# Optimization experiments

Measured on AMD Instinct MI355X. Metric: run time of the kernel, lower is better.

Reference implementation:

```python
import jax, jax.numpy as jnp
import numpy as np

N_NODES = 50000
N_EDGES = 800000
N_GRAPHS = 128
IN_DIM = 12          # state_ndim + action_ndim
C = 64               # n_channels
N_LAYERS = 2
NEG_SLOPE = 0.01     # torch leaky_relu default


def setup_inputs() -> dict:
    key = jax.random.key(0)
    ks = jax.random.split(key, 16)
    state = jax.random.normal(ks[0], (N_NODES, 8), dtype=jnp.float32)
    action = jax.random.normal(ks[1], (N_NODES, 4), dtype=jnp.float32)
    edge_index = jax.random.randint(ks[2], (2, N_EDGES), 0, N_NODES, dtype=jnp.int64)
    edge_attr = jax.random.normal(ks[3], (N_EDGES, IN_DIM), dtype=jnp.float32)
    batch = jnp.sort(jax.random.randint(ks[4], (N_NODES,), 0, N_GRAPHS, dtype=jnp.int64))
    s = 0.05
    params = {
        "W_in": jax.random.normal(ks[5], (IN_DIM, C), dtype=jnp.float32) * s,
        "b_in": jnp.zeros((C,), dtype=jnp.float32),
        "W_self": jax.random.normal(ks[6], (N_LAYERS, C, C), dtype=jnp.float32) * s,
        "W_nbr": jax.random.normal(ks[7], (N_LAYERS, C, C), dtype=jnp.float32) * s,
        "W_edge": jax.random.normal(ks[8], (N_LAYERS, IN_DIM, C), dtype=jnp.float32) * s,
        "b_conv": jnp.zeros((N_LAYERS, C), dtype=jnp.float32),
        "W_out": jax.random.normal(ks[9], (C, 1), dtype=jnp.float32) * s,
        "b_out": jnp.zeros((1,), dtype=jnp.float32),
    }
    return {"state": state, "action": action, "edge_index": edge_index,
            "edge_attr": edge_attr, "batch": batch, **params}


def reference(state, action, edge_index, edge_attr, batch,
              W_in, b_in, W_self, W_nbr, W_edge, b_conv, W_out, b_out):
    N = state.shape[0]
    src, dst = edge_index[0], edge_index[1]
    act = lambda v: jax.nn.leaky_relu(v, NEG_SLOPE)

    # read-in: concat state/action -> node embedding [N, C]
    x = jnp.concatenate([state, action], axis=-1)
    h = act(x @ W_in + b_in)

    # message passing: gather -> transform -> scatter-add, edge_attr-conditioned
    for l in range(W_self.shape[0]):
        m = h[src] @ W_nbr[l] + edge_attr @ W_edge[l]          # [E, C]
        agg = jax.ops.segment_sum(m, dst, num_segments=N)      # [N, C]
        h = act(h @ W_self[l] + agg + b_conv[l])

    # read-out to scalar per node, then scatter_mean over graph ids
    y = h @ W_out + b_out                                      # [N, 1]
    sums = jax.ops.segment_sum(y, batch, num_segments=N_GRAPHS)
    counts = jax.ops.segment_sum(jnp.ones((N, 1), y.dtype), batch,
                                 num_segments=N_GRAPHS)
    return sums / jnp.maximum(counts, 1.0)                     # [B, 1]
```

## Files before the change

### kernel.cpp

```cpp
#include <hip/hip_runtime.h>

#define NN 50000
#define NE 800000
#define NG 128
#define IN_DIM 12
#define C 64
#define KTOT 160
#define NEG_SLOPE 0.01f
#define SCAN_BLOCKS 196
#define NOWN 8
#define OWN_RANGE 6250
#define ESTRIPE 2048
#define NSTRIPES ((NE + ESTRIPE - 1) / ESTRIPE)

typedef short short8 __attribute__((ext_vector_type(8)));
typedef float f32x4 __attribute__((ext_vector_type(4)));
typedef unsigned int uint4v __attribute__((ext_vector_type(4)));

__device__ __forceinline__ float lrelu(float v) {
    return v > 0.f ? v : NEG_SLOPE * v;
}
__device__ __forceinline__ float bflo(uint32_t v) { return __uint_as_float(v << 16); }
__device__ __forceinline__ float bfhi(uint32_t v) { return __uint_as_float(v & 0xffff0000u); }
__device__ __forceinline__ unsigned short bf16r(float x) {
    uint32_t u = __float_as_uint(x);
    u += 0x7fffu + ((u >> 16) & 1u);
    return (unsigned short)(u >> 16);
}
__device__ __forceinline__ uint32_t pack_bf16(float lo, float hi) {
    return (uint32_t)bf16r(lo) | ((uint32_t)bf16r(hi) << 16);
}

__global__ void readin_kernel(const float* __restrict__ state,
                              const float* __restrict__ action,
                              const float* __restrict__ W_in,
                              const float* __restrict__ b_in,
                              uint32_t* __restrict__ hb) {
    __shared__ float sW[IN_DIM * C];
    __shared__ float sb[C];
    int tid = threadIdx.x;
    for (int i = tid; i < IN_DIM * C; i += blockDim.x) sW[i] = W_in[i];
    if (tid < C) sb[tid] = b_in[tid];
    __syncthreads();

    int node = blockIdx.x * (blockDim.x >> 6) + (tid >> 6);
    int c = tid & 63;
    if (node >= NN) return;

    float x[IN_DIM];
#pragma unroll
    for (int k = 0; k < 8; k++) x[k] = state[node * 8 + k];
#pragma unroll
    for (int k = 0; k < 4; k++) x[8 + k] = action[node * 4 + k];

    float acc = sb[c];
#pragma unroll
    for (int k = 0; k < IN_DIM; k++) acc += x[k] * sW[k * C + c];
    float res = lrelu(acc);
    float p = __shfl_xor(res, 1);
    if (!(c & 1)) hb[node * 32 + (c >> 1)] = pack_bf16(res, p);
}

__global__ void hist_part(const int* __restrict__ dst, int* __restrict__ deg) {
    int owner = blockIdx.x & (NOWN - 1);
    int stripe = blockIdx.x >> 3;
    int lo = owner * OWN_RANGE, hi = lo + OWN_RANGE;
    int base = stripe * ESTRIPE;
    int end = base + ESTRIPE; if (end > NE) end = NE;
    for (int e = base + threadIdx.x; e < end; e += 256) {
        int d = dst[e];
        if (d >= lo && d < hi) atomicAdd(&deg[d], 1);
    }
}

__global__ void scan1_kernel(const int* __restrict__ deg,
                             int* __restrict__ excl,
                             int* __restrict__ bsum) {
    __shared__ int tmp[256];
    int tid = threadIdx.x;
    int i = blockIdx.x * 256 + tid;
    int v = (i < NN) ? deg[i] : 0;
    tmp[tid] = v;
    __syncthreads();
    for (int off = 1; off < 256; off <<= 1) {
        int t = (tid >= off) ? tmp[tid - off] : 0;
        __syncthreads();
        tmp[tid] += t;
        __syncthreads();
    }
    if (i < NN) excl[i] = tmp[tid] - v;
    if (tid == 255) bsum[blockIdx.x] = tmp[255];
}

__global__ void scan23_kernel(const int* __restrict__ excl,
                              const int* __restrict__ bsum,
                              int* __restrict__ row_start,
                              int* __restrict__ cursor) {
    __shared__ int s_off;
    int tid = threadIdx.x;
    if (tid < 64) {
        int p = 0;
        for (int i = tid; i < blockIdx.x; i += 64) p += bsum[i];
#pragma unroll
        for (int off = 32; off; off >>= 1) p += __shfl_xor(p, off);
        if (tid == 0) s_off = p;
    }
    __syncthreads();
    int i = blockIdx.x * 256 + tid;
    if (i < NN) {
        int v = excl[i] + s_off;
        row_start[i] = v;
        cursor[i] = v;
    }
}

__global__ void fill_part(const int* __restrict__ src,
                          const int* __restrict__ dst,
                          const float* __restrict__ edge_attr,
                          int* __restrict__ cursor,
                          int* __restrict__ csr_src,
                          uint4v* __restrict__ csr_ea) {
    int owner = blockIdx.x & (NOWN - 1);
    int stripe = blockIdx.x >> 3;
    int lo = owner * OWN_RANGE, hi = lo + OWN_RANGE;
    int base = stripe * ESTRIPE;
    int end = base + ESTRIPE; if (end > NE) end = NE;
    for (int e = base + threadIdx.x; e < end; e += 256) {
        int d = dst[e];
        if (d >= lo && d < hi) {
            int slot = atomicAdd(&cursor[d], 1);
            csr_src[slot] = src[e];
            const float4* ea = reinterpret_cast<const float4*>(edge_attr + e * IN_DIM);
            float4 f0 = ea[0], f1 = ea[1], f2 = ea[2];
            uint4v w0, w1;
            w0[0] = pack_bf16(f0.x, f0.y); w0[1] = pack_bf16(f0.z, f0.w);
            w0[2] = pack_bf16(f1.x, f1.y); w0[3] = pack_bf16(f1.z, f1.w);
            w1[0] = pack_bf16(f2.x, f2.y); w1[1] = pack_bf16(f2.z, f2.w);
            w1[2] = 0u; w1[3] = 0u;
            csr_ea[slot * 2] = w0;
            csr_ea[slot * 2 + 1] = w1;
        }
    }
}

__global__ void wprep_kernel(const float* __restrict__ W_self,
                             const float* __restrict__ W_nbr,
                             const float* __restrict__ W_edge,
                             unsigned short* __restrict__ WT) {
    int idx = blockIdx.x * 256 + threadIdx.x;
    if (idx >= 2 * C * KTOT) return;
    int l = idx / (C * KTOT);
    int rem = idx % (C * KTOT);
    int col = rem / KTOT;
    int k = rem % KTOT;
    float v = 0.f;
    if (k < C)                    v = W_self[l * C * C + k * C + col];
    else if (k < 2 * C)           v = W_nbr[l * C * C + (k - C) * C + col];
    else if (k < 2 * C + IN_DIM)  v = W_edge[l * IN_DIM * C + (k - 2 * C) * C + col];
    WT[idx] = bf16r(v);
}

__global__ void agg_e_kernel(const uint32_t* __restrict__ csr_ea,
                             const int* __restrict__ row_start,
                             const int* __restrict__ deg,
                             uint32_t* __restrict__ aggeb) {
    int tid = threadIdx.x;
    int node = blockIdx.x * (blockDim.x >> 6) + (tid >> 6);
    int lane = tid & 63;
    if (node >= NN) return;
    int start = row_start[node], cnt = deg[node];
    int eg = lane >> 3;
    int comp = lane & 7;
    float s0 = 0.f, s1 = 0.f;
    for (int j = eg; j < cnt; j += 8) {
        uint32_t v = csr_ea[(size_t)(start + j) * 8 + comp];
        s0 += bflo(v); s1 += bfhi(v);
    }
    s0 += __shfl_xor(s0, 8);  s1 += __shfl_xor(s1, 8);
    s0 += __shfl_xor(s0, 16); s1 += __shfl_xor(s1, 16);
    s0 += __shfl_xor(s0, 32); s1 += __shfl_xor(s1, 32);
    if (lane < 8) aggeb[node * 8 + comp] = pack_bf16(s0, s1);
}

__global__ void gather_kernel(const uint32_t* __restrict__ hb_in,
                              const int* __restrict__ row_start,
                              const int* __restrict__ deg,
                              const int* __restrict__ csr_src,
                              uint32_t* __restrict__ aggb) {
    int tid = threadIdx.x;
    int node = blockIdx.x * (blockDim.x >> 6) + (tid >> 6);
    int lane = tid & 63;
    if (node >= NN) return;

    int start = row_start[node], cnt = deg[node];
    int half = lane >> 5;
    int q = lane & 31;

    int myidx = (lane < cnt) ? csr_src[start + lane] : 0;
    int nb = cnt < 64 ? cnt : 64;

    float a0 = 0.f, a1 = 0.f, b0v = 0.f, b1v = 0.f;
    float c0 = 0.f, c1 = 0.f, d0 = 0.f, d1 = 0.f;
    int j = 0;
    for (; j + 16 <= nb; j += 16) {
        int p = j + 4 * half;
        int s0 = __shfl(myidx, p);
        int s1 = __shfl(myidx, p + 1);
        int s2 = __shfl(myidx, p + 2);
        int s3 = __shfl(myidx, p + 3);
        int s4 = __shfl(myidx, p + 8);
        int s5 = __shfl(myidx, p + 9);
        int s6 = __shfl(myidx, p + 10);
        int s7 = __shfl(myidx, p + 11);
        uint32_t v0 = hb_in[s0 * 32 + q];
        uint32_t v1 = hb_in[s1 * 32 + q];
        uint32_t v2 = hb_in[s2 * 32 + q];
        uint32_t v3 = hb_in[s3 * 32 + q];
        uint32_t v4 = hb_in[s4 * 32 + q];
        uint32_t v5 = hb_in[s5 * 32 + q];
        uint32_t v6 = hb_in[s6 * 32 + q];
        uint32_t v7 = hb_in[s7 * 32 + q];
        a0  += bflo(v0); a1  += bfhi(v0);
        b0v += bflo(v1); b1v += bfhi(v1);
        c0  += bflo(v2); c1  += bfhi(v2);
        d0  += bflo(v3); d1  += bfhi(v3);
        a0  += bflo(v4); a1  += bfhi(v4);
        b0v += bflo(v5); b1v += bfhi(v5);
        c0  += bflo(v6); c1  += bfhi(v6);
        d0  += bflo(v7); d1  += bfhi(v7);
    }
    for (; j + 8 <= nb; j += 8) {
        int p = j + 4 * half;
        int s0 = __shfl(myidx, p);
        int s1 = __shfl(myidx, p + 1);
        int s2 = __shfl(myidx, p + 2);
        int s3 = __shfl(myidx, p + 3);
        uint32_t v0 = hb_in[s0 * 32 + q];
        uint32_t v1 = hb_in[s1 * 32 + q];
        uint32_t v2 = hb_in[s2 * 32 + q];
        uint32_t v3 = hb_in[s3 * 32 + q];
        a0  += bflo(v0); a1  += bfhi(v0);
        b0v += bflo(v1); b1v += bfhi(v1);
        c0  += bflo(v2); c1  += bfhi(v2);
        d0  += bflo(v3); d1  += bfhi(v3);
    }
    for (; j + 2 <= nb; j += 2) {
        int s = __shfl(myidx, j + half);
        uint32_t v = hb_in[s * 32 + q];
        a0 += bflo(v); a1 += bfhi(v);
    }
    {
        int s = __shfl(myidx, (j < 64) ? j : 0);
        if (j < nb && half == 0) {
            uint32_t v = hb_in[s * 32 + q];
            a0 += bflo(v); a1 += bfhi(v);
        }
    }
    for (int i2 = 64 + half; i2 < cnt; i2 += 2) {
        int s = csr_src[start + i2];
        uint32_t v = hb_in[s * 32 + q];
        a0 += bflo(v); a1 += bfhi(v);
    }
    a0 += b0v + c0 + d0;
    a1 += b1v + c1 + d1;
    a0 += __shfl_xor(a0, 32);
    a1 += __shfl_xor(a1, 32);
    if (lane < 32) aggb[node * 32 + q] = pack_bf16(a0, a1);
}

__global__ __launch_bounds__(512) void gemm_kernel(
        const uint32_t* __restrict__ hbA,
        const uint32_t* __restrict__ aggb,
        const uint32_t* __restrict__ aggeb,
        const unsigned short* __restrict__ WT,
        const float* __restrict__ bias,
        unsigned short* __restrict__ hb_out) {
    int tid = threadIdx.x;
    int w = tid >> 6;
    int l = tid & 63;
    int mt = blockIdx.x * 2 + (w >> 2);
    if (mt * 16 >= NN) return;
    int nt = w & 3;
    int node_base = mt * 16;

    int arow = l & 15;
    int kg = l >> 4;
    int gcol = nt * 16 + arow;

    const uint32_t* aptr = hbA + (node_base + arow) * 32 + kg * 4;
    const uint32_t* gptr = aggb + (node_base + arow) * 32 + kg * 4;
    short8 a0 = __builtin_bit_cast(short8, *reinterpret_cast<const uint4v*>(aptr));
    short8 a1 = __builtin_bit_cast(short8, *reinterpret_cast<const uint4v*>(aptr + 16));
    short8 a2 = __builtin_bit_cast(short8, *reinterpret_cast<const uint4v*>(gptr));
    short8 a3 = __builtin_bit_cast(short8, *reinterpret_cast<const uint4v*>(gptr + 16));
    short8 a4 = {0, 0, 0, 0, 0, 0, 0, 0};
    if (kg < 2)
        a4 = __builtin_bit_cast(short8, *reinterpret_cast<const uint4v*>(
                 aggeb + (node_base + arow) * 8 + kg * 4));

    const unsigned short* bbase = WT + gcol * KTOT + kg * 8;
    short8 b0 = __builtin_bit_cast(short8, *reinterpret_cast<const uint4v*>(bbase));
    short8 b1 = __builtin_bit_cast(short8, *reinterpret_cast<const uint4v*>(bbase + 32));
    short8 b2 = __builtin_bit_cast(short8, *reinterpret_cast<const uint4v*>(bbase + 64));
    short8 b3 = __builtin_bit_cast(short8, *reinterpret_cast<const uint4v*>(bbase + 96));
    short8 b4 = __builtin_bit_cast(short8, *reinterpret_cast<const uint4v*>(bbase + 128));

    float bv = bias[gcol];
    f32x4 acc = {bv, bv, bv, bv};

    acc = __builtin_amdgcn_mfma_f32_16x16x32_bf16(a0, b0, acc, 0, 0, 0);
    acc = __builtin_amdgcn_mfma_f32_16x16x32_bf16(a1, b1, acc, 0, 0, 0);
    acc = __builtin_amdgcn_mfma_f32_16x16x32_bf16(a2, b2, acc, 0, 0, 0);
    acc = __builtin_amdgcn_mfma_f32_16x16x32_bf16(a3, b3, acc, 0, 0, 0);
    acc = __builtin_amdgcn_mfma_f32_16x16x32_bf16(a4, b4, acc, 0, 0, 0);

#pragma unroll
    for (int r = 0; r < 4; r++) {
        float res = lrelu(acc[r]);
        hb_out[(node_base + kg * 4 + r) * C + gcol] = bf16r(res);
    }
}

__global__ void readout_fused(const unsigned short* __restrict__ hb,
                              const float* __restrict__ W_out,
                              const float* __restrict__ b_out,
                              const int* __restrict__ batch,
                              float* __restrict__ sums,
                              float* __restrict__ counts) {
    __shared__ float s_sum[NG];
    __shared__ float s_cnt[NG];
    int tid = threadIdx.x;
    if (tid < NG) { s_sum[tid] = 0.f; s_cnt[tid] = 0.f; }
    __syncthreads();

    int lane = tid & 63;
    int wave = tid >> 6;
    int base = blockIdx.x * 256 + wave * 64;
    float w = W_out[lane];
    float b0 = b_out[0];

    if (base < NN) {
        int last = base + 63;
        bool full = (last < NN);
        int gf = batch[base];
        int gl = batch[full ? last : (NN - 1)];
        if (full && gf == gl) {
            float p = 0.f;
            for (int i = 0; i < 64; i++)
                p += __uint_as_float((uint32_t)hb[(base + i) * C + lane] << 16);
            p *= w;
#pragma unroll
            for (int off = 32; off; off >>= 1) p += __shfl_xor(p, off);
            if (lane == 0) {
                atomicAdd(&s_sum[gf], p + 64.f * b0);
                atomicAdd(&s_cnt[gf], 64.f);
            }
        } else {
            float y_local = 0.f;
            for (int i = 0; i < 64; i++) {
                int nd = base + i;
                float v = 0.f;
                if (nd < NN) v = __uint_as_float((uint32_t)hb[nd * C + lane] << 16) * w;
#pragma unroll
                for (int off = 32; off; off >>= 1) v += __shfl_xor(v, off);
                if (lane == i) y_local = v + b0;
            }
            int nd = base + lane;
            if (nd < NN) {
                int g = batch[nd];
                atomicAdd(&s_sum[g], y_local);
                atomicAdd(&s_cnt[g], 1.0f);
            }
        }
    }
    __syncthreads();
    if (tid < NG && s_cnt[tid] != 0.f) {
        atomicAdd(&sums[tid], s_sum[tid]);
        atomicAdd(&counts[tid], s_cnt[tid]);
    }
}

__global__ void finalize_kernel(const float* __restrict__ sums,
                                const float* __restrict__ counts,
                                float* __restrict__ out) {
    int g = threadIdx.x;
    if (g < NG) out[g] = sums[g] / fmaxf(counts[g], 1.0f);
}

extern "C" void kernel_launch(void* const* d_in, const int* in_sizes, int n_in,
                              void* d_out, int out_size, void* d_ws, size_t ws_size,
                              hipStream_t stream) {
    const float* state     = (const float*)d_in[0];
    const float* action    = (const float*)d_in[1];
    const int*   edge_index= (const int*)d_in[2];
    const float* edge_attr = (const float*)d_in[3];
    const int*   batch     = (const int*)d_in[4];
    const float* W_in      = (const float*)d_in[5];
    const float* b_in      = (const float*)d_in[6];
    const float* W_self    = (const float*)d_in[7];
    const float* W_nbr     = (const float*)d_in[8];
    const float* W_edge    = (const float*)d_in[9];
    const float* b_conv    = (const float*)d_in[10];
    const float* W_out     = (const float*)d_in[11];
    const float* b_out     = (const float*)d_in[12];
    float* out = (float*)d_out;

    const int* src = edge_index;
    const int* dst = edge_index + NE;

    float* ws      = (float*)d_ws;
    float* sums    = ws;
    float* counts  = sums + NG;
    int*   deg     = (int*)(counts + NG);
    int*   excl    = deg + NN;
    int*   row_start = excl + NN;
    int*   cursor  = row_start + NN;
    int*   bsum    = cursor + NN;
    int*   csr_src = bsum + 256;
    uint32_t* csr_ea = (uint32_t*)(csr_src + NE);
    uint32_t* hb_a = csr_ea + (size_t)NE * 8;
    uint32_t* hb_b = hb_a + NN * 32;
    uint32_t* aggb = hb_b + NN * 32;
    uint32_t* aggeb = aggb + NN * 32;
    unsigned short* WT = (unsigned short*)(aggeb + NN * 8);

    hipMemsetAsync(deg, 0, NN * sizeof(int), stream);
    hipMemsetAsync(sums, 0, 2 * NG * sizeof(float), stream);

    const int THREADS = 256;
    int node_blocks = (NN + 3) / 4;
    int part_blocks = NSTRIPES * NOWN;

    readin_kernel<<<node_blocks, THREADS, 0, stream>>>(state, action, W_in, b_in, hb_a);

    hist_part<<<part_blocks, THREADS, 0, stream>>>(dst, deg);
    scan1_kernel<<<SCAN_BLOCKS, 256, 0, stream>>>(deg, excl, bsum);
    scan23_kernel<<<SCAN_BLOCKS, 256, 0, stream>>>(excl, bsum, row_start, cursor);
    fill_part<<<part_blocks, THREADS, 0, stream>>>(src, dst, edge_attr, cursor,
                                                   csr_src, (uint4v*)csr_ea);

    wprep_kernel<<<80, 256, 0, stream>>>(W_self, W_nbr, W_edge, WT);

    agg_e_kernel<<<node_blocks, THREADS, 0, stream>>>(csr_ea, row_start, deg, aggeb);

    int gemm_blocks = (3125 + 1) / 2;

    gather_kernel<<<node_blocks, THREADS, 0, stream>>>(hb_a, row_start, deg, csr_src, aggb);
    gemm_kernel<<<gemm_blocks, 512, 0, stream>>>(
        hb_a, aggb, aggeb, WT, b_conv, (unsigned short*)hb_b);

    gather_kernel<<<node_blocks, THREADS, 0, stream>>>(hb_b, row_start, deg, csr_src, aggb);
    gemm_kernel<<<gemm_blocks, 512, 0, stream>>>(
        hb_b, aggb, aggeb, WT + C * KTOT, b_conv + C, (unsigned short*)hb_a);

    int ro_blocks = (NN + 255) / 256;
    readout_fused<<<ro_blocks, THREADS, 0, stream>>>(
        (const unsigned short*)hb_a, W_out, b_out, batch, sums, counts);
    finalize_kernel<<<1, 128, 0, stream>>>(sums, counts, out);
}
```

Measured before the change: 335.6 us.

## Pack edge attrs separately, store edge ids in CSR, fuse edge aggregation into gather

Edge attributes are now packed to bf16 in edge order by a separate coalesced kernel, instead of being scattered into CSR slots during the atomic fill. The fill only writes (src, edge id) pairs. The per-node edge-attribute sum moves into the first gather kernel, which reads the packed attributes indirectly through the edge ids. This cuts scattered 32-byte writes in the fill and removes one launch, at the cost of random 24-byte reads of edge attributes during the gather and a wider CSR index entry that both gathers must read.

```diff
diff --git a/kernel.cpp b/kernel.cpp
--- a/kernel.cpp
+++ b/kernel.cpp
@@ -61,6 +61,19 @@
     if (!(c & 1)) hb[node * 32 + (c >> 1)] = pack_bf16(res, p);
 }
 
+__global__ void pack_kernel(const float* __restrict__ edge_attr,
+                            uint32_t* __restrict__ ea6) {
+    int e = blockIdx.x * 256 + threadIdx.x;
+    if (e >= NE) return;
+    const float4* ea = reinterpret_cast<const float4*>(edge_attr + (size_t)e * IN_DIM);
+    float4 f0 = ea[0], f1 = ea[1], f2 = ea[2];
+    uint2* o = reinterpret_cast<uint2*>(ea6 + (size_t)e * 6);
+    uint2 t;
+    t.x = pack_bf16(f0.x, f0.y); t.y = pack_bf16(f0.z, f0.w); o[0] = t;
+    t.x = pack_bf16(f1.x, f1.y); t.y = pack_bf16(f1.z, f1.w); o[1] = t;
+    t.x = pack_bf16(f2.x, f2.y); t.y = pack_bf16(f2.z, f2.w); o[2] = t;
+}
+
 __global__ void hist_part(const int* __restrict__ dst, int* __restrict__ deg) {
     int owner = blockIdx.x & (NOWN - 1);
     int stripe = blockIdx.x >> 3;
@@ -116,10 +129,8 @@
 
 __global__ void fill_part(const int* __restrict__ src,
                           const int* __restrict__ dst,
-                          const float* __restrict__ edge_attr,
                           int* __restrict__ cursor,
-                          int* __restrict__ csr_src,
-                          uint4v* __restrict__ csr_ea) {
+                          int2* __restrict__ csr2) {
     int owner = blockIdx.x & (NOWN - 1);
     int stripe = blockIdx.x >> 3;
     int lo = owner * OWN_RANGE, hi = lo + OWN_RANGE;
@@ -129,16 +140,7 @@
         int d = dst[e];
         if (d >= lo && d < hi) {
             int slot = atomicAdd(&cursor[d], 1);
-            csr_src[slot] = src[e];
-            const float4* ea = reinterpret_cast<const float4*>(edge_attr + e * IN_DIM);
-            float4 f0 = ea[0], f1 = ea[1], f2 = ea[2];
-            uint4v w0, w1;
-            w0[0] = pack_bf16(f0.x, f0.y); w0[1] = pack_bf16(f0.z, f0.w);
-            w0[2] = pack_bf16(f1.x, f1.y); w0[3] = pack_bf16(f1.z, f1.w);
-            w1[0] = pack_bf16(f2.x, f2.y); w1[1] = pack_bf16(f2.z, f2.w);
-            w1[2] = 0u; w1[3] = 0u;
-            csr_ea[slot * 2] = w0;
-            csr_ea[slot * 2 + 1] = w1;
+            csr2[slot] = make_int2(src[e], e);
         }
     }
 }
@@ -160,43 +162,24 @@
     WT[idx] = bf16r(v);
 }
 
-__global__ void agg_e_kernel(const uint32_t* __restrict__ csr_ea,
-                             const int* __restrict__ row_start,
-                             const int* __restrict__ deg,
-                             uint32_t* __restrict__ aggeb) {
+__global__ void gather_kernel(const uint32_t* __restrict__ hb_in,
+                              const int* __restrict__ row_start,
+                              const int* __restrict__ deg,
+                              const int2* __restrict__ csr2,
+                              const uint32_t* __restrict__ ea6,
+                              uint32_t* __restrict__ aggb,
+                              uint32_t* __restrict__ aggeb,
+                              int doea) {
     int tid = threadIdx.x;
     int node = blockIdx.x * (blockDim.x >> 6) + (tid >> 6);
     int lane = tid & 63;
     if (node >= NN) return;
-    int start = row_start[node], cnt = deg[node];
-    int eg = lane >> 3;
-    int comp = lane & 7;
-    float s0 = 0.f, s1 = 0.f;
-    for (int j = eg; j < cnt; j += 8) {
-        uint32_t v = csr_ea[(size_t)(start + j) * 8 + comp];
-        s0 += bflo(v); s1 += bfhi(v);
-    }
-    s0 += __shfl_xor(s0, 8);  s1 += __shfl_xor(s1, 8);
-    s0 += __shfl_xor(s0, 16); s1 += __shfl_xor(s1, 16);
-    s0 += __shfl_xor(s0, 32); s1 += __shfl_xor(s1, 32);
-    if (lane < 8) aggeb[node * 8 + comp] = pack_bf16(s0, s1);
-}
-
-__global__ void gather_kernel(const uint32_t* __restrict__ hb_in,
-                              const int* __restrict__ row_start,
-                              const int* __restrict__ deg,
-                              const int* __restrict__ csr_src,
-                              uint32_t* __restrict__ aggb) {
-    int tid = threadIdx.x;
-    int node = blockIdx.x * (blockDim.x >> 6) + (tid >> 6);
-    int lane = tid & 63;
-    if (node >= NN) return;
 
     int start = row_start[node], cnt = deg[node];
     int half = lane >> 5;
     int q = lane & 31;
 
-    int myidx = (lane < cnt) ? csr_src[start + lane] : 0;
+    int myidx = (lane < cnt) ? csr2[start + lane].x : 0;
     int nb = cnt < 64 ? cnt : 64;
 
     float a0 = 0.f, a1 = 0.f, b0v = 0.f, b1v = 0.f;
@@ -257,10 +240,28 @@
         }
     }
     for (int i2 = 64 + half; i2 < cnt; i2 += 2) {
-        int s = csr_src[start + i2];
+        int s = csr2[start + i2].x;
         uint32_t v = hb_in[s * 32 + q];
         a0 += bflo(v); a1 += bfhi(v);
     }
+
+    if (doea) {
+        int g = lane >> 3;
+        int comp = lane & 7;
+        float e0 = 0.f, e1 = 0.f;
+        for (int j2 = g; j2 < cnt; j2 += 8) {
+            int eid = csr2[start + j2].y;
+            if (comp < 6) {
+                uint32_t v = ea6[(size_t)eid * 6 + comp];
+                e0 += bflo(v); e1 += bfhi(v);
+            }
+        }
+        e0 += __shfl_xor(e0, 8);  e1 += __shfl_xor(e1, 8);
+        e0 += __shfl_xor(e0, 16); e1 += __shfl_xor(e1, 16);
+        e0 += __shfl_xor(e0, 32); e1 += __shfl_xor(e1, 32);
+        if (lane < 8) aggeb[node * 8 + lane] = (lane < 6) ? pack_bf16(e0, e1) : 0u;
+    }
+
     a0 += b0v + c0 + d0;
     a1 += b1v + c1 + d1;
     a0 += __shfl_xor(a0, 32);
@@ -416,9 +417,9 @@
     int*   row_start = excl + NN;
     int*   cursor  = row_start + NN;
     int*   bsum    = cursor + NN;
-    int*   csr_src = bsum + 256;
-    uint32_t* csr_ea = (uint32_t*)(csr_src + NE);
-    uint32_t* hb_a = csr_ea + (size_t)NE * 8;
+    int2*  csr2    = (int2*)(bsum + 256);
+    uint32_t* ea6  = (uint32_t*)(csr2 + NE);
+    uint32_t* hb_a = ea6 + (size_t)NE * 6;
     uint32_t* hb_b = hb_a + NN * 32;
     uint32_t* aggb = hb_b + NN * 32;
     uint32_t* aggeb = aggb + NN * 32;
@@ -430,26 +431,27 @@
     const int THREADS = 256;
     int node_blocks = (NN + 3) / 4;
     int part_blocks = NSTRIPES * NOWN;
+    int pack_blocks = (NE + THREADS - 1) / THREADS;
 
     readin_kernel<<<node_blocks, THREADS, 0, stream>>>(state, action, W_in, b_in, hb_a);
+    pack_kernel<<<pack_blocks, THREADS, 0, stream>>>(edge_attr, ea6);
 
     hist_part<<<part_blocks, THREADS, 0, stream>>>(dst, deg);
     scan1_kernel<<<SCAN_BLOCKS, 256, 0, stream>>>(deg, excl, bsum);
     scan23_kernel<<<SCAN_BLOCKS, 256, 0, stream>>>(excl, bsum, row_start, cursor);
-    fill_part<<<part_blocks, THREADS, 0, stream>>>(src, dst, edge_attr, cursor,
-                                                   csr_src, (uint4v*)csr_ea);
+    fill_part<<<part_blocks, THREADS, 0, stream>>>(src, dst, cursor, csr2);
 
     wprep_kernel<<<80, 256, 0, stream>>>(W_self, W_nbr, W_edge, WT);
 
-    agg_e_kernel<<<node_blocks, THREADS, 0, stream>>>(csr_ea, row_start, deg, aggeb);
-
     int gemm_blocks = (3125 + 1) / 2;
 
-    gather_kernel<<<node_blocks, THREADS, 0, stream>>>(hb_a, row_start, deg, csr_src, aggb);
+    gather_kernel<<<node_blocks, THREADS, 0, stream>>>(
+        hb_a, row_start, deg, csr2, ea6, aggb, aggeb, 1);
     gemm_kernel<<<gemm_blocks, 512, 0, stream>>>(
         hb_a, aggb, aggeb, WT, b_conv, (unsigned short*)hb_b);
 
-    gather_kernel<<<node_blocks, THREADS, 0, stream>>>(hb_b, row_start, deg, csr_src, aggb);
+    gather_kernel<<<node_blocks, THREADS, 0, stream>>>(
+        hb_b, row_start, deg, csr2, ea6, aggb, aggeb, 0);
     gemm_kernel<<<gemm_blocks, 512, 0, stream>>>(
         hb_b, aggb, aggeb, WT + C * KTOT, b_conv + C, (unsigned short*)hb_a);
 
```

After: 327.3 us. -2.5%, faster.
